# Kernel tuning notes

Measured on AMD Instinct MI355X. Metric: run time of the kernel, lower is better.

## Reference

```python
import jax, jax.numpy as jnp
import numpy as np

B, S, C, H = 4096, 31, 512, 8  # seq_len fixed at num_particles+1 = 31 by the module
HD = C // H
EPS = 1e-5


def setup_inputs() -> dict:
    key = jax.random.key(0)
    ks = jax.random.split(key, 10)
    rn = lambda k, sh: jax.random.normal(k, sh, dtype=jnp.float32)
    scale = 1.0 / np.sqrt(C)
    return {
        "x": rn(ks[0], (B, S, C)),
        "norm_w": 1.0 + 0.1 * rn(ks[1], (C,)),
        "norm_b": 0.1 * rn(ks[2], (C,)),
        "Wq": rn(ks[3], (C, C)) * scale,
        "Wk": rn(ks[4], (C, C)) * scale,
        "Wv": rn(ks[5], (C, C)) * scale,
        "Wout": rn(ks[6], (C, C)) * scale,
        "b_out": 0.1 * rn(ks[7], (C,)),
        "pen_w": 1.0 + 0.1 * rn(ks[8], (S * S,)),
        "pen_b": 0.1 * rn(ks[9], (S * S,)),
    }


def reference(x, norm_w, norm_b, Wq, Wk, Wv, Wout, b_out, pen_w, pen_b):
    # BatchNorm1d(in_dim) applied to x.transpose(1,2): per-channel stats over (batch, seq).
    # Training-mode BN: biased variance, eps=1e-5.
    mu = jnp.mean(x, axis=(0, 1))
    var = jnp.var(x, axis=(0, 1))
    xn = (x - mu) * jax.lax.rsqrt(var + EPS) * norm_w + norm_b

    # QKV projections (Linear, no bias): y = x @ W.T
    q = (xn @ Wq.T).reshape(B, S, H, HD)
    k = (xn @ Wk.T).reshape(B, S, H, HD)
    v = (xn @ Wv.T).reshape(B, S, H, HD)

    # energy: [B, H, S, S]
    energy = jnp.einsum("nqhc,nkhc->nhqk", q, k)

    # BatchNorm1d(S*S) on energy.view(B,H,S*S).transpose(1,2):
    # per-(q,k)-position stats over (batch, heads).
    mu2 = jnp.mean(energy, axis=(0, 1))   # [S, S]
    var2 = jnp.var(energy, axis=(0, 1))   # [S, S]
    en = (energy - mu2) * jax.lax.rsqrt(var2 + EPS)
    en = en * pen_w.reshape(S, S) + pen_b.reshape(S, S)

    attn = jax.nn.softmax(en / jnp.sqrt(jnp.float32(C)), axis=-1)

    out = jnp.einsum("nhql,nlhc->nqhc", attn, v).reshape(B, S, C)
    return out @ Wout.T + b_out + x
```

## Files before the change

kernel.cpp:

```cpp
#include <hip/hip_runtime.h>

typedef unsigned short u16;
typedef unsigned int   u32;
typedef __attribute__((ext_vector_type(4))) float f32x4;
typedef __attribute__((ext_vector_type(8))) short bf16x8;

#define BB 4096
#define SS 31
#define CC 512
#define HH 8
#define MM (BB*SS)
#define NPAIR (BB*HH)
#define SSQ (SS*SS)

__device__ __forceinline__ u16 f2bf(float f){
  union { float f; u32 u; } v; v.f = f;
  u32 r = (v.u + 0x7fffu + ((v.u >> 16) & 1u)) >> 16;
  return (u16)r;
}
__device__ __forceinline__ float bf2f(u16 u){
  union { u32 u; float f; } v; v.u = ((u32)u) << 16;
  return v.f;
}
__device__ __forceinline__ void gload_lds16(const u16* g, u16* l){
  __builtin_amdgcn_global_load_lds((const __attribute__((address_space(1))) void*)g,
                                   (__attribute__((address_space(3))) void*)l, 16, 0, 0);
}

__global__ __launch_bounds__(512) void bn1_stats_k(const float* __restrict__ x, float* __restrict__ acc){
  int c = threadIdx.x;
  float s = 0.f, q = 0.f;
  for (int r = blockIdx.x; r < MM; r += gridDim.x){
    float v = x[(long)r*CC + c];
    s += v; q += v*v;
  }
  atomicAdd(&acc[c], s);
  atomicAdd(&acc[CC + c], q);
}

__global__ __launch_bounds__(512) void bn1_final_k(const float* __restrict__ acc, const float* __restrict__ w,
                                                   const float* __restrict__ b, float* __restrict__ scsh){
  int c = threadIdx.x;
  const float invN = 1.f / (float)MM;
  float mu  = acc[c] * invN;
  float var = acc[CC+c] * invN - mu*mu;
  float rs  = rsqrtf(var + 1e-5f);
  float sc  = w[c] * rs;
  scsh[c]    = sc;
  scsh[CC+c] = b[c] - mu*sc;
}

__global__ __launch_bounds__(256) void bn1_apply_k(const float* __restrict__ x, const float* __restrict__ scsh,
                                                   u16* __restrict__ xn){
  const int tot = MM*CC/8;
  int stride = gridDim.x * blockDim.x;
  for (int i = blockIdx.x*blockDim.x + threadIdx.x; i < tot; i += stride){
    const f32x4* xp = (const f32x4*)x;
    f32x4 a = xp[2l*i], b2 = xp[2l*i+1];
    int c = (i*8) & (CC-1);
    u16 r[8];
    #pragma unroll
    for (int j = 0; j < 4; j++) r[j]   = f2bf(a[j] *scsh[c+j]   + scsh[CC+c+j]);
    #pragma unroll
    for (int j = 0; j < 4; j++) r[4+j] = f2bf(b2[j]*scsh[c+4+j] + scsh[CC+c+4+j]);
    *(bf16x8*)(xn + 8l*i) = *(bf16x8*)r;
  }
}

__global__ __launch_bounds__(256) void wconv_k(const float* __restrict__ a, const float* __restrict__ b,
                                               const float* __restrict__ c, const float* __restrict__ d,
                                               u16* __restrict__ o){
  int i = blockIdx.x*256 + threadIdx.x;
  if (i >= 4*CC*CC) return;
  int w = i >> 18;
  const float* src = w==0 ? a : (w==1 ? b : (w==2 ? c : d));
  o[i] = f2bf(src[i & (CC*CC-1)]);
}

template<int FINAL>
__global__ __launch_bounds__(256) void gemm_bt_k(
    const u16* __restrict__ A,
    const u16* __restrict__ W0, const u16* __restrict__ W1, const u16* __restrict__ W2,
    u16* __restrict__ O0, u16* __restrict__ O1, u16* __restrict__ O2,
    const float* __restrict__ bias, const float* __restrict__ resid, float* __restrict__ out)
{
  __shared__ u16 As[128*64];
  __shared__ u16 Bs[128*64];
  const int t  = threadIdx.x;
  const int mt = blockIdx.y * 128;
  int ntile;
  const u16* Wsel; u16* Osel = nullptr;
  if (FINAL) { Wsel = W0; ntile = blockIdx.x; }
  else {
    int wi = blockIdx.x >> 2; ntile = blockIdx.x & 3;
    Wsel = wi==0 ? W0 : (wi==1 ? W1 : W2);
    Osel = wi==0 ? O0 : (wi==1 ? O1 : O2);
  }
  const u16* Ab = A    + (long)mt*CC;
  const u16* Bb = Wsel + (long)ntile*128*CC;
  const int lane = t & 63, wv = t >> 6;
  const int wr = wv >> 1, wc = wv & 1;
  const int lr = lane & 15, hi = lane >> 4;
  const int srow = t >> 3, scg = t & 7;

  f32x4 acc[4][4];
  #pragma unroll
  for (int m=0;m<4;m++)
    #pragma unroll
    for (int n=0;n<4;n++)
      acc[m][n] = (f32x4){0.f,0.f,0.f,0.f};

  for (int kk = 0; kk < CC; kk += 64){
    #pragma unroll
    for (int s2 = 0; s2 < 4; s2++){
      int r2 = srow + 32*s2;
      gload_lds16(Ab + (long)r2*CC + kk + scg*8, &As[r2*64 + scg*8]);
      gload_lds16(Bb + (long)r2*CC + kk + scg*8, &Bs[r2*64 + scg*8]);
    }
    __syncthreads();
    #pragma unroll
    for (int ks = 0; ks < 2; ks++){
      bf16x8 af[4], bfr[4];
      #pragma unroll
      for (int m=0;m<4;m++) af[m]  = *(const bf16x8*)&As[(wr*64 + m*16 + lr)*64 + ks*32 + hi*8];
      #pragma unroll
      for (int n=0;n<4;n++) bfr[n] = *(const bf16x8*)&Bs[(wc*64 + n*16 + lr)*64 + ks*32 + hi*8];
      #pragma unroll
      for (int m=0;m<4;m++)
        #pragma unroll
        for (int n=0;n<4;n++)
          acc[m][n] = __builtin_amdgcn_mfma_f32_16x16x32_bf16(af[m], bfr[n], acc[m][n], 0, 0, 0);
    }
    __syncthreads();
  }
  #pragma unroll
  for (int m=0;m<4;m++){
    int gr = mt + wr*64 + m*16 + hi*4;
    #pragma unroll
    for (int n=0;n<4;n++){
      int gc = ntile*128 + wc*64 + n*16 + lr;
      #pragma unroll
      for (int j=0;j<4;j++){
        long off = (long)(gr + j)*CC + gc;
        if (FINAL) out[off] = acc[m][n][j] + bias[gc] + resid[off];
        else       Osel[off] = f2bf(acc[m][n][j]);
      }
    }
  }
}

__global__ __launch_bounds__(256) void energy_k(const u16* __restrict__ q, const u16* __restrict__ k,
                                                float* __restrict__ e){
  const int wv = threadIdx.x >> 6, lane = threadIdx.x & 63;
  const int lr = lane & 15, hi = lane >> 4;
  #pragma unroll 1
  for (int it = 0; it < 4; it++){
    int p = blockIdx.x*4 + wv + 8192*it;
    int b = p >> 3, h = p & 7;
    long base = ((long)b*SS)*CC + h*64;
    bf16x8 aq[2][2], ak[2][2];
    #pragma unroll
    for (int m=0;m<2;m++){
      int s = m*16 + lr;
      #pragma unroll
      for (int ks=0;ks<2;ks++){
        bf16x8 z = {0,0,0,0,0,0,0,0};
        aq[m][ks] = z; ak[m][ks] = z;
        if (s < SS){
          aq[m][ks] = *(const bf16x8*)&q[base + (long)s*CC + ks*32 + hi*8];
          ak[m][ks] = *(const bf16x8*)&k[base + (long)s*CC + ks*32 + hi*8];
        }
      }
    }
    f32x4 acc[2][2];
    #pragma unroll
    for (int m=0;m<2;m++)
      #pragma unroll
      for (int n=0;n<2;n++)
        acc[m][n] = (f32x4){0.f,0.f,0.f,0.f};
    #pragma unroll
    for (int ks=0;ks<2;ks++)
      #pragma unroll
      for (int m=0;m<2;m++)
        #pragma unroll
        for (int n=0;n<2;n++)
          acc[m][n] = __builtin_amdgcn_mfma_f32_16x16x32_bf16(aq[m][ks], ak[n][ks], acc[m][n], 0, 0, 0);
    long eb = (long)p*SSQ;
    #pragma unroll
    for (int m=0;m<2;m++)
      #pragma unroll
      for (int n=0;n<2;n++)
        #pragma unroll
        for (int j=0;j<4;j++){
          int s = m*16 + hi*4 + j, s2 = n*16 + lr;
          if (s < SS && s2 < SS) e[eb + s*SS + s2] = acc[m][n][j];
        }
  }
}

__global__ __launch_bounds__(256) void bn2_stats_k(const float* __restrict__ e, float* __restrict__ acc2){
  int p = blockIdx.x*256 + threadIdx.x;
  if (p >= SSQ) return;
  float s = 0.f, q = 0.f;
  int r0 = blockIdx.y * 128;
  for (int r = r0; r < r0 + 128; r++){
    float v = e[(long)r*SSQ + p];
    s += v; q += v*v;
  }
  atomicAdd(&acc2[p], s);
  atomicAdd(&acc2[1024 + p], q);
}

__global__ __launch_bounds__(256) void bn2_final_k(const float* __restrict__ acc2, const float* __restrict__ pw,
                                                   const float* __restrict__ pb, float* __restrict__ ss2){
  int p = blockIdx.x*256 + threadIdx.x;
  if (p >= SSQ) return;
  const float invN = 1.f/32768.f;
  const float invs = 0.04419417382415922f;
  float mu  = acc2[p]*invN;
  float var = acc2[1024+p]*invN - mu*mu;
  float rs  = rsqrtf(var + 1e-5f);
  float srp = rs * pw[p];
  ss2[p]      = srp * invs;
  ss2[1024+p] = (pb[p] - mu*srp) * invs;
}

__global__ __launch_bounds__(256) void attn_pv_k(const float* __restrict__ e, const float* __restrict__ ss2,
                                                 const u16* __restrict__ v, u16* __restrict__ ctx){
  __shared__ float sc2[SSQ], sh2[SSQ];
  __shared__ float att[4][SSQ];
  for (int i = threadIdx.x; i < SSQ; i += 256){ sc2[i] = ss2[i]; sh2[i] = ss2[1024+i]; }
  __syncthreads();
  const int wv = threadIdx.x >> 6, lane = threadIdx.x & 63;
  #pragma unroll 1
  for (int it = 0; it < 4; it++){
    int p = blockIdx.x*4 + wv + 8192*it;
    int b = p >> 3, h = p & 7;
    long eb = (long)p*SSQ;
    for (int i = lane; i < SSQ; i += 64)
      att[wv][i] = e[eb + i]*sc2[i] + sh2[i];
    __syncthreads();
    if (lane < SS){
      int ro = lane*SS;
      float mx = -1e30f;
      for (int j=0;j<SS;j++) mx = fmaxf(mx, att[wv][ro + j]);
      float sum = 0.f;
      for (int j=0;j<SS;j++) sum += __expf(att[wv][ro + j] - mx);
      float inv = 1.f / sum;
      for (int j=0;j<SS;j++) att[wv][ro + j] = __expf(att[wv][ro + j] - mx) * inv;
    }
    __syncthreads();
    long vbase = ((long)b*SS)*CC + h*64 + lane;
    float vr[SS];
    #pragma unroll
    for (int j=0;j<SS;j++) vr[j] = bf2f(v[vbase + (long)j*CC]);
    #pragma unroll 1
    for (int s=0;s<SS;s++){
      float c = 0.f;
      #pragma unroll
      for (int j=0;j<SS;j++) c += att[wv][s*SS + j] * vr[j];
      ctx[vbase + (long)s*CC] = f2bf(c);
    }
    __syncthreads();
  }
}

extern "C" void kernel_launch(void* const* d_in, const int* in_sizes, int n_in,
                              void* d_out, int out_size, void* d_ws, size_t ws_size,
                              hipStream_t stream)
{
  const float* x      = (const float*)d_in[0];
  const float* norm_w = (const float*)d_in[1];
  const float* norm_b = (const float*)d_in[2];
  const float* Wq     = (const float*)d_in[3];
  const float* Wk     = (const float*)d_in[4];
  const float* Wv     = (const float*)d_in[5];
  const float* Wout   = (const float*)d_in[6];
  const float* b_out  = (const float*)d_in[7];
  const float* pen_w  = (const float*)d_in[8];
  const float* pen_b  = (const float*)d_in[9];
  float* out = (float*)d_out;

  char* ws = (char*)d_ws;
  const size_t WQB   = 0;
  const size_t STATS = 2097152;
  const size_t SCSH1 = STATS + 16384;
  const size_t SS2O  = SCSH1 + 4096;
  const size_t BIG0  = 2129920;
  const size_t BIGSZ = 130023424;
  u16*   wq    = (u16*)(ws + WQB);
  float* stats = (float*)(ws + STATS);
  float* acc2  = (float*)(ws + STATS + 4096);
  float* scsh  = (float*)(ws + SCSH1);
  float* ss2   = (float*)(ws + SS2O);
  u16*   xn    = (u16*)(ws + BIG0);
  float* e     = (float*)(ws + BIG0);
  u16*   qb    = (u16*)(ws + BIG0 + BIGSZ);
  u16*   kb    = (u16*)(ws + BIG0 + 2*BIGSZ);
  u16*   vb    = (u16*)(ws + BIG0 + 3*BIGSZ);
  u16*   ctx   = qb;

  (void)hipMemsetAsync(ws + STATS, 0, 16384, stream);
  wconv_k<<<4096, 256, 0, stream>>>(Wq, Wk, Wv, Wout, wq);
  bn1_stats_k<<<512, 512, 0, stream>>>(x, stats);
  bn1_final_k<<<1, 512, 0, stream>>>(stats, norm_w, norm_b, scsh);
  bn1_apply_k<<<2048, 256, 0, stream>>>(x, scsh, xn);
  gemm_bt_k<0><<<dim3(12, 992), 256, 0, stream>>>(xn, wq, wq + 262144, wq + 2*262144,
                                                  qb, kb, vb, nullptr, nullptr, nullptr);
  energy_k<<<2048, 256, 0, stream>>>(qb, kb, e);
  bn2_stats_k<<<dim3(4, 256), 256, 0, stream>>>(e, acc2);
  bn2_final_k<<<4, 256, 0, stream>>>(acc2, pen_w, pen_b, ss2);
  attn_pv_k<<<2048, 256, 0, stream>>>(e, ss2, vb, ctx);
  gemm_bt_k<1><<<dim3(4, 992), 256, 0, stream>>>(ctx, wq + 3*262144, nullptr, nullptr,
                                                 nullptr, nullptr, nullptr, b_out, x, out);
}
```

Baseline: 1.299 ms.

## Rewrite projection GEMMs with 256x256 tiles and triple-buffered async LDS pipeline

Replaces the 128x128 single-buffered GEMM with a 256x256-tile, 512-thread kernel. It uses a three-stage ring of LDS buffers filled by global_load_lds with explicit vmcnt waits, so loads for step k+2 overlap MFMA work on step k. A 16-byte XOR swizzle on the LDS layout reduces bank conflicts, and s_setprio raises priority around the MFMA burst. Larger tiles double per-block data reuse, at the cost of more registers (32 accumulators per wave), fewer blocks, and fragile hand-written waitcnt and barrier sequencing.

```diff
diff --git a/kernel.cpp b/kernel.cpp
--- a/kernel.cpp
+++ b/kernel.cpp
@@ -10,7 +10,6 @@
 #define CC 512
 #define HH 8
 #define MM (BB*SS)
-#define NPAIR (BB*HH)
 #define SSQ (SS*SS)
 
 __device__ __forceinline__ u16 f2bf(float f){
@@ -78,67 +77,90 @@
 }
 
 template<int FINAL>
-__global__ __launch_bounds__(256) void gemm_bt_k(
+__global__ __launch_bounds__(512,2) void gemm256_k(
     const u16* __restrict__ A,
     const u16* __restrict__ W0, const u16* __restrict__ W1, const u16* __restrict__ W2,
     u16* __restrict__ O0, u16* __restrict__ O1, u16* __restrict__ O2,
     const float* __restrict__ bias, const float* __restrict__ resid, float* __restrict__ out)
 {
-  __shared__ u16 As[128*64];
-  __shared__ u16 Bs[128*64];
+  __shared__ u16 lds[3*16384];
   const int t  = threadIdx.x;
-  const int mt = blockIdx.y * 128;
-  int ntile;
-  const u16* Wsel; u16* Osel = nullptr;
-  if (FINAL) { Wsel = W0; ntile = blockIdx.x; }
+  const int mt = blockIdx.y * 256;
+  int nt; const u16* Wsel; u16* Osel = nullptr;
+  if (FINAL) { Wsel = W0; nt = blockIdx.x; }
   else {
-    int wi = blockIdx.x >> 2; ntile = blockIdx.x & 3;
+    int wi = blockIdx.x >> 1; nt = blockIdx.x & 1;
     Wsel = wi==0 ? W0 : (wi==1 ? W1 : W2);
     Osel = wi==0 ? O0 : (wi==1 ? O1 : O2);
   }
   const u16* Ab = A    + (long)mt*CC;
-  const u16* Bb = Wsel + (long)ntile*128*CC;
-  const int lane = t & 63, wv = t >> 6;
-  const int wr = wv >> 1, wc = wv & 1;
+  const u16* Bb = Wsel + (long)nt*256*CC;
+  const int lane = t & 63;
+  const int wv = t >> 6, wm = wv >> 2, wn = wv & 3;
   const int lr = lane & 15, hi = lane >> 4;
-  const int srow = t >> 3, scg = t & 7;
-
-  f32x4 acc[4][4];
+  const int srow = t >> 2;
+  const int sc   = t & 3;
+  const int sg   = sc ^ ((t >> 3) & 3);
+
+  f32x4 acc[8][4];
   #pragma unroll
-  for (int m=0;m<4;m++)
+  for (int m=0;m<8;m++)
     #pragma unroll
     for (int n=0;n<4;n++)
       acc[m][n] = (f32x4){0.f,0.f,0.f,0.f};
 
-  for (int kk = 0; kk < CC; kk += 64){
-    #pragma unroll
-    for (int s2 = 0; s2 < 4; s2++){
-      int r2 = srow + 32*s2;
-      gload_lds16(Ab + (long)r2*CC + kk + scg*8, &As[r2*64 + scg*8]);
-      gload_lds16(Bb + (long)r2*CC + kk + scg*8, &Bs[r2*64 + scg*8]);
-    }
-    __syncthreads();
-    #pragma unroll
-    for (int ks = 0; ks < 2; ks++){
-      bf16x8 af[4], bfr[4];
-      #pragma unroll
-      for (int m=0;m<4;m++) af[m]  = *(const bf16x8*)&As[(wr*64 + m*16 + lr)*64 + ks*32 + hi*8];
-      #pragma unroll
-      for (int n=0;n<4;n++) bfr[n] = *(const bf16x8*)&Bs[(wc*64 + n*16 + lr)*64 + ks*32 + hi*8];
-      #pragma unroll
-      for (int m=0;m<4;m++)
-        #pragma unroll
-        for (int n=0;n<4;n++)
-          acc[m][n] = __builtin_amdgcn_mfma_f32_16x16x32_bf16(af[m], bfr[n], acc[m][n], 0, 0, 0);
-    }
-    __syncthreads();
-  }
+  auto STAGE = [&](int kt){
+    u16* Al = &lds[(kt % 3) * 16384];
+    u16* Bl = Al + 8192;
+    const u16* As = Ab + (long)srow*CC + kt*32 + sg*8;
+    const u16* Bs = Bb + (long)srow*CC + kt*32 + sg*8;
+    gload_lds16(As,          &Al[srow*32 + sc*8]);
+    gload_lds16(As + 128*CC, &Al[(srow+128)*32 + sc*8]);
+    gload_lds16(Bs,          &Bl[srow*32 + sc*8]);
+    gload_lds16(Bs + 128*CC, &Bl[(srow+128)*32 + sc*8]);
+  };
+
+  STAGE(0); STAGE(1);
+  asm volatile("s_waitcnt vmcnt(4)" ::: "memory");
+  asm volatile("s_barrier" ::: "memory");
+
+  const int chR = hi ^ ((lr >> 1) & 3);
+  #pragma unroll 1
+  for (int kt = 0; kt < 16; ++kt){
+    if (kt < 14) STAGE(kt + 2);
+    const u16* Al = &lds[(kt % 3) * 16384];
+    const u16* Bl = Al + 8192;
+    bf16x8 af[8], bfr[4];
+    #pragma unroll
+    for (int m=0;m<8;m++){
+      int row = wm*128 + m*16 + lr;
+      af[m] = *(const bf16x8*)&Al[row*32 + chR*8];
+    }
+    #pragma unroll
+    for (int n=0;n<4;n++){
+      int row = wn*64 + n*16 + lr;
+      bfr[n] = *(const bf16x8*)&Bl[row*32 + chR*8];
+    }
+    asm volatile("s_waitcnt lgkmcnt(0)" ::: "memory");
+    __builtin_amdgcn_sched_barrier(0);
+    __builtin_amdgcn_s_setprio(1);
+    #pragma unroll
+    for (int m=0;m<8;m++)
+      #pragma unroll
+      for (int n=0;n<4;n++)
+        acc[m][n] = __builtin_amdgcn_mfma_f32_16x16x32_bf16(af[m], bfr[n], acc[m][n], 0, 0, 0);
+    __builtin_amdgcn_s_setprio(0);
+    if (kt < 14)       asm volatile("s_waitcnt vmcnt(4)" ::: "memory");
+    else if (kt == 14) asm volatile("s_waitcnt vmcnt(0)" ::: "memory");
+    if (kt < 15)       asm volatile("s_barrier" ::: "memory");
+  }
+
   #pragma unroll
-  for (int m=0;m<4;m++){
-    int gr = mt + wr*64 + m*16 + hi*4;
+  for (int m=0;m<8;m++){
+    int gr = mt + wm*128 + m*16 + hi*4;
     #pragma unroll
     for (int n=0;n<4;n++){
-      int gc = ntile*128 + wc*64 + n*16 + lr;
+      int gc = nt*256 + wn*64 + n*16 + lr;
       #pragma unroll
       for (int j=0;j<4;j++){
         long off = (long)(gr + j)*CC + gc;
@@ -305,12 +327,12 @@
   bn1_stats_k<<<512, 512, 0, stream>>>(x, stats);
   bn1_final_k<<<1, 512, 0, stream>>>(stats, norm_w, norm_b, scsh);
   bn1_apply_k<<<2048, 256, 0, stream>>>(x, scsh, xn);
-  gemm_bt_k<0><<<dim3(12, 992), 256, 0, stream>>>(xn, wq, wq + 262144, wq + 2*262144,
-                                                  qb, kb, vb, nullptr, nullptr, nullptr);
+  gemm256_k<0><<<dim3(6, 496), 512, 0, stream>>>(xn, wq, wq + 262144, wq + 2*262144,
+                                                 qb, kb, vb, nullptr, nullptr, nullptr);
   energy_k<<<2048, 256, 0, stream>>>(qb, kb, e);
   bn2_stats_k<<<dim3(4, 256), 256, 0, stream>>>(e, acc2);
   bn2_final_k<<<4, 256, 0, stream>>>(acc2, pen_w, pen_b, ss2);
   attn_pv_k<<<2048, 256, 0, stream>>>(e, ss2, vb, ctx);
-  gemm_bt_k<1><<<dim3(4, 992), 256, 0, stream>>>(ctx, wq + 3*262144, nullptr, nullptr,
+  gemm256_k<1><<<dim3(2, 496), 512, 0, stream>>>(ctx, wq + 3*262144, nullptr, nullptr,
                                                  nullptr, nullptr, nullptr, b_out, x, out);
 }
```

New measurement: 1.235 ms. -5.0%, faster.
